# Kernel optimization log

Hardware: AMD Instinct MI355X
Metric: run time of the kernel (lower is better)

## Reference

```python
import math
import jax, jax.numpy as jnp
import numpy as np

D = 128
F = 512
EPS = 1e-5

def _lin(x, W, b):
    return x @ W + b  # W: [in, out]

def _bn(x2d, gamma, beta):
    # BatchNorm1d with track_running_stats=False: always batch stats, biased var
    m = jnp.mean(x2d, axis=0)
    v = jnp.mean((x2d - m) ** 2, axis=0)
    return gamma * (x2d - m) / jnp.sqrt(v + EPS) + beta

def _gelu(x):
    c = math.sqrt(2.0 / math.pi)
    return 0.5 * x * (1.0 + jnp.tanh(c * (x + 0.044715 * x ** 3)))

def setup_inputs() -> dict:
    key = jax.random.key(0)
    ks = jax.random.split(key, 16)
    B, N = 8, 256
    s = 1.0 / math.sqrt(D)
    inp = {
        'h': jax.random.normal(ks[0], (B, N, D), jnp.float32),
        'e': jax.random.normal(ks[1], (B, N, N, D), jnp.float32),
        'Uw': jax.random.uniform(ks[2], (D, D), jnp.float32, -s, s), 'Ub': jnp.zeros((D,), jnp.float32),
        'Vw': jax.random.uniform(ks[3], (D, D), jnp.float32, -s, s), 'Vb': jnp.zeros((D,), jnp.float32),
        'Aw': jax.random.uniform(ks[4], (D, D), jnp.float32, -s, s), 'Ab': jnp.zeros((D,), jnp.float32),
        'Bw': jax.random.uniform(ks[5], (D, D), jnp.float32, -s, s), 'Bb': jnp.zeros((D,), jnp.float32),
        'Cw': jax.random.uniform(ks[6], (D, D), jnp.float32, -s, s), 'Cb': jnp.zeros((D,), jnp.float32),
        'gamma_h': jnp.ones((D,), jnp.float32), 'beta_h': jnp.zeros((D,), jnp.float32),
        'gamma_e': jnp.ones((D,), jnp.float32), 'beta_e': jnp.zeros((D,), jnp.float32),
        'W1': jax.random.uniform(ks[7], (D, F), jnp.float32, -s, s), 'b1': jnp.zeros((F,), jnp.float32),
        'W2': jax.random.uniform(ks[8], (F, D), jnp.float32, -1.0 / math.sqrt(F), 1.0 / math.sqrt(F)), 'b2': jnp.zeros((D,), jnp.float32),
    }
    return inp

def reference(h, e, Uw, Ub, Vw, Vb, Aw, Ab, Bw, Bb, Cw, Cb,
              gamma_h, beta_h, gamma_e, beta_e, W1, b1, W2, b2):
    B, N, Dd = h.shape
    h_in, e_in = h, e
    Uh = _lin(h, Uw, Ub)          # [B,N,D]
    Vh = _lin(h, Vw, Vb)          # [B,N,D]
    Ah = _lin(h, Aw, Ab)
    Bh = _lin(h, Bw, Bb)
    Ce = _lin(e, Cw, Cb)          # [B,N,N,D]
    e_new = Ah[:, None, :, :] + Bh[:, :, None, :] + Ce  # [B,N,N,D]
    gates = jax.nn.sigmoid(e_new)
    # sum_j gates[b,i,j,d] * Vh[b,j,d]
    h_new = Uh + jnp.einsum('bijd,bjd->bid', gates, Vh)
    h_new = _bn(h_new.reshape(B * N, Dd), gamma_h, beta_h).reshape(B, N, Dd)
    e_out = _bn(e_new.reshape(B * N * N, Dd), gamma_e, beta_e).reshape(B, N, N, Dd)
    e_out = jax.nn.relu(e_out)
    h_new = _lin(_gelu(_lin(h_new, W1, b1)), W2, b2)
    return (h_in + h_new, e_in + e_out)
```

## Files before the change

### kernel.cpp

```cpp
#include <hip/hip_runtime.h>
#include <math.h>

#define D 128
#define NN 256
#define NB 2048
#define FF 512

typedef float f32x4 __attribute__((ext_vector_type(4)));
typedef __bf16 bf16x8 __attribute__((ext_vector_type(8)));
typedef unsigned int u32x4 __attribute__((ext_vector_type(4)));

__device__ __forceinline__ float gelu_f(float x) {
  float x3 = x * x * x;
  float u = 0.7978845608028654f * (x + 0.044715f * x3);
  return 0.5f * x * (1.0f + tanhf(u));
}

__device__ __forceinline__ bf16x8 cvt8(f32x4 a, f32x4 b) {
  bf16x8 r;
  r[0] = (__bf16)a.x; r[1] = (__bf16)a.y; r[2] = (__bf16)a.z; r[3] = (__bf16)a.w;
  r[4] = (__bf16)b.x; r[5] = (__bf16)b.y; r[6] = (__bf16)b.z; r[7] = (__bf16)b.w;
  return r;
}

__device__ __forceinline__ float sigmoid_f(float v) {
  float ex = __builtin_amdgcn_exp2f(-1.44269504f * v);
  return __builtin_amdgcn_rcpf(1.0f + ex);
}

__device__ __forceinline__ unsigned int packbf(float a, float v) {
  unsigned short ha = __builtin_bit_cast(unsigned short, (__bf16)a);
  unsigned short hv = __builtin_bit_cast(unsigned short, (__bf16)v);
  return (unsigned int)ha | ((unsigned int)hv << 16);
}
__device__ __forceinline__ float bflo(unsigned int u) {
  return __builtin_bit_cast(float, u << 16);
}
__device__ __forceinline__ float bfhi(unsigned int u) {
  return __builtin_bit_cast(float, u & 0xffff0000u);
}

__global__ __launch_bounds__(256) void k0_pack(const float* __restrict__ Cw,
                                               __bf16* __restrict__ ws0) {
  int tid = blockIdx.x * 256 + threadIdx.x;
  int l  = tid & 63;
  int nt = tid >> 8;
  int ks = (tid >> 6) & 3;
  int d  = nt * 16 + (l & 15);
  int kb = ks * 32 + (l >> 4) * 8;
  bf16x8 v;
#pragma unroll
  for (int q = 0; q < 8; ++q) v[q] = (__bf16)Cw[(kb + q) * D + d];
  *(bf16x8*)(ws0 + tid * 8) = v;
}

__global__ __launch_bounds__(256) void k1_lin4(
    const float* __restrict__ h,
    const float* __restrict__ Uw, const float* __restrict__ Ub,
    const float* __restrict__ Vw, const float* __restrict__ Vb,
    const float* __restrict__ Aw, const float* __restrict__ Ab,
    const float* __restrict__ Bw, const float* __restrict__ Bb,
    const float* __restrict__ Cb,
    float* __restrict__ wsU, float* __restrict__ wsB,
    unsigned int* __restrict__ wsAVT, unsigned int* __restrict__ wsAVR) {
  __shared__ float hrow[D];
  __shared__ float exA[D];
  __shared__ float exV[D];
  int row = blockIdx.x;
  int b = row >> 8, i = row & 255;
  int t = threadIdx.x;
  if (t < D) hrow[t] = h[row * D + t];
  __syncthreads();
  int d = t & 127;
  bool lo = (t < 128);
  const float* W0 = lo ? Uw : Vw;
  const float* W1m = lo ? Aw : Bw;
  float a0 = (lo ? Ub : Vb)[d];
  float a1 = lo ? Ab[d] : (Bb[d] + Cb[d]);
#pragma unroll 4
  for (int k = 0; k < D; ++k) {
    float hk = hrow[k];
    a0 = fmaf(hk, W0[k * D + d], a0);
    a1 = fmaf(hk, W1m[k * D + d], a1);
  }
  if (lo) {
    wsU[row * D + d] = a0;
    exA[d] = a1;
  } else {
    exV[d] = a0;
    wsB[row * D + d] = a1;
  }
  __syncthreads();
  if (t < 128) {
    unsigned int p = packbf(exA[t], exV[t]);
    wsAVR[row * D + t] = p;
    wsAVT[(b << 15) + t * NN + i] = p;
  }
}

__global__ __launch_bounds__(256, 3) void k_gemm(
    const float* __restrict__ e,
    const __bf16* __restrict__ ws0,
    __bf16* __restrict__ ws1) {
  __shared__ __align__(16) __bf16 bfr[16384];
  __shared__ __align__(16) unsigned int stW[4224];
  const int t = threadIdx.x;
  const int blk = blockIdx.x;

#pragma unroll
  for (int c = 0; c < 8; ++c) {
    int idx = c * 256 + t;
    *(f32x4*)(bfr + idx * 8) = *(const f32x4*)(ws0 + idx * 8);
  }
  __syncthreads();

  const int w = t >> 6;
  const int l = t & 63;
  const int l15 = l & 15;
  const int lhi = l >> 4;
  unsigned int* stWu = stW + w * 1056;

  const float* eblk = e + (size_t)blk * (NN * D);

  const float* ap = eblk + (w * 64 + l15) * D + lhi * 8;
  f32x4 pf[8];
#pragma unroll
  for (int q = 0; q < 8; ++q) pf[q] = *(const f32x4*)(ap + (q >> 1) * 32 + (q & 1) * 4);

#pragma unroll 1
  for (int mt = 0; mt < 4; ++mt) {
    bf16x8 af[4];
#pragma unroll
    for (int ks = 0; ks < 4; ++ks) af[ks] = cvt8(pf[2 * ks], pf[2 * ks + 1]);
    if (mt < 3) {
      const float* ap2 = ap + (mt + 1) * 16 * D;
#pragma unroll
      for (int q = 0; q < 8; ++q) pf[q] = *(const f32x4*)(ap2 + (q >> 1) * 32 + (q & 1) * 4);
    }
    const int J0 = w * 64 + mt * 16;
#pragma unroll
    for (int nt = 0; nt < 8; ++nt) {
      f32x4 acc = {0.f, 0.f, 0.f, 0.f};
#pragma unroll
      for (int ks = 0; ks < 4; ++ks) {
        bf16x8 bfrg = *(const bf16x8*)(bfr + ((nt * 4 + ks) * 64 + l) * 8);
        acc = __builtin_amdgcn_mfma_f32_16x16x32_bf16(af[ks], bfrg, acc, 0, 0, 0);
      }
#pragma unroll
      for (int r = 0; r < 4; ++r) {
        float v = acc[r];
        float vp = __shfl_xor(v, 1);
        if ((l15 & 1) == 0) {
          stWu[(lhi * 4 + r) * 66 + (nt << 3) + (l15 >> 1)] = packbf(v, vp);
        }
      }
    }
    unsigned int* dstu = (unsigned int*)(ws1 + (size_t)blk * (NN * D) + J0 * D);
#pragma unroll
    for (int i = 0; i < 16; ++i) {
      dstu[i * 64 + l] = stWu[i * 66 + l];
    }
  }
}

__global__ __launch_bounds__(256) void k_stats(
    const __bf16* __restrict__ ws1,
    const unsigned int* __restrict__ AVR,
    const float* __restrict__ Bh2,
    float* __restrict__ wsP) {
  __shared__ float red[16][3][128];
  const int t = threadIdx.x;
  const int blk = blockIdx.x;
  const int b = blk >> 8;
  const int jg = t >> 4;
  const int dg = t & 15;

  float cb[8];
  {
    f32x4 c0 = *(const f32x4*)(Bh2 + blk * D + dg * 8);
    f32x4 c1 = *(const f32x4*)(Bh2 + blk * D + dg * 8 + 4);
#pragma unroll
    for (int q = 0; q < 4; ++q) { cb[q] = c0[q]; cb[4 + q] = c1[q]; }
  }

  float es[8], eq[8], hp[8];
#pragma unroll
  for (int q = 0; q < 8; ++q) { es[q] = 0.f; eq[q] = 0.f; hp[q] = 0.f; }

  const unsigned int* w1 = (const unsigned int*)(ws1 + (size_t)blk * (NN * D));
  const unsigned int* avb = AVR + ((size_t)(b << 8)) * D;

#pragma unroll 1
  for (int k = 0; k < 16; ++k) {
    const int j = k * 16 + jg;
    u32x4 a = *(const u32x4*)(w1 + j * 64 + dg * 4);
    u32x4 av0 = *(const u32x4*)(avb + j * D + dg * 8);
    u32x4 av1 = *(const u32x4*)(avb + j * D + dg * 8 + 4);
#pragma unroll
    for (int q = 0; q < 4; ++q) {
      unsigned int avA = (q < 2) ? av0[2 * q] : av1[2 * (q - 2)];
      unsigned int avB = (q < 2) ? av0[2 * q + 1] : av1[2 * (q - 2) + 1];
      float v0 = bflo(a[q]) + cb[2 * q] + bflo(avA);
      float v1 = bfhi(a[q]) + cb[2 * q + 1] + bflo(avB);
      es[2 * q] += v0;
      eq[2 * q] = fmaf(v0, v0, eq[2 * q]);
      hp[2 * q] = fmaf(sigmoid_f(v0), bfhi(avA), hp[2 * q]);
      es[2 * q + 1] += v1;
      eq[2 * q + 1] = fmaf(v1, v1, eq[2 * q + 1]);
      hp[2 * q + 1] = fmaf(sigmoid_f(v1), bfhi(avB), hp[2 * q + 1]);
    }
  }

#pragma unroll
  for (int q = 0; q < 8; ++q) {
    red[jg][0][dg * 8 + q] = es[q];
    red[jg][1][dg * 8 + q] = eq[q];
    red[jg][2][dg * 8 + q] = hp[q];
  }
  __syncthreads();
  if (t < 128) {
    float S = 0.f, Q = 0.f, H = 0.f;
#pragma unroll
    for (int g = 0; g < 16; ++g) {
      S += red[g][0][t];
      Q += red[g][1][t];
      H += red[g][2][t];
    }
    wsP[blk * 384 + t] = S;
    wsP[blk * 384 + 128 + t] = Q;
    wsP[blk * 384 + 256 + t] = H;
  }
}

__global__ __launch_bounds__(256) void k_epass1s(
    const __bf16* __restrict__ ws1,
    const float* __restrict__ e,
    const unsigned int* __restrict__ AVR,
    const float* __restrict__ Bh2,
    const float* __restrict__ ws6,
    float* __restrict__ out_e) {
  const int tid = blockIdx.x * 256 + threadIdx.x;
  const int d0 = (tid & 15) * 8;
  f32x4 ge0 = *(const f32x4*)(ws6 + d0);
  f32x4 ge1 = *(const f32x4*)(ws6 + d0 + 4);
  f32x4 be0 = *(const f32x4*)(ws6 + 128 + d0);
  f32x4 be1 = *(const f32x4*)(ws6 + 128 + d0 + 4);
#pragma unroll 2
  for (int k = 0; k < 16; ++k) {
    size_t idx = (size_t)tid + (size_t)k * 524288;
    size_t row = idx >> 4;
    int j = (int)(row & 255);
    int bb = (int)(row >> 16);
    size_t avrow = ((size_t)(bb << 8) + j);
    u32x4 u = *(const u32x4*)(ws1 + idx * 8);
    u32x4 av0 = *(const u32x4*)(AVR + avrow * D + d0);
    u32x4 av1 = *(const u32x4*)(AVR + avrow * D + d0 + 4);
    const float* cbp = Bh2 + (row >> 8) * D + d0;
    f32x4 c0 = *(const f32x4*)cbp;
    f32x4 c1 = *(const f32x4*)(cbp + 4);
    const float* ep = e + idx * 8;
    f32x4 e0 = *(const f32x4*)ep;
    f32x4 e1 = *(const f32x4*)(ep + 4);
    f32x4 o0, o1;
#pragma unroll
    for (int q = 0; q < 2; ++q) {
      float v0 = bflo(u[q]) + c0[2 * q] + bflo(av0[2 * q]);
      float v1 = bfhi(u[q]) + c0[2 * q + 1] + bflo(av0[2 * q + 1]);
      o0[2 * q]     = fmaxf(fmaf(v0, ge0[2 * q], be0[2 * q]), 0.f) + e0[2 * q];
      o0[2 * q + 1] = fmaxf(fmaf(v1, ge0[2 * q + 1], be0[2 * q + 1]), 0.f) + e0[2 * q + 1];
      float v2 = bflo(u[2 + q]) + c1[2 * q] + bflo(av1[2 * q]);
      float v3 = bfhi(u[2 + q]) + c1[2 * q + 1] + bflo(av1[2 * q + 1]);
      o1[2 * q]     = fmaxf(fmaf(v2, ge1[2 * q], be1[2 * q]), 0.f) + e1[2 * q];
      o1[2 * q + 1] = fmaxf(fmaf(v3, ge1[2 * q + 1], be1[2 * q + 1]), 0.f) + e1[2 * q + 1];
    }
    float* op = out_e + idx * 8;
    *(f32x4*)op = o0;
    *(f32x4*)(op + 4) = o1;
  }
}

__global__ __launch_bounds__(256, 3) void k_epass0_fused(
    const float* __restrict__ e,
    const __bf16* __restrict__ ws0,
    const unsigned int* __restrict__ AVT,
    const float* __restrict__ Bh2,
    float* __restrict__ wsP) {
  __shared__ __align__(16) __bf16 bfr[16384];
  __shared__ __align__(16) unsigned int uni32[4224];
  const int t = threadIdx.x;
  const int blk = blockIdx.x;
  const int b = blk >> 8;

#pragma unroll
  for (int c = 0; c < 8; ++c) {
    int idx = c * 256 + t;
    *(f32x4*)(bfr + idx * 8) = *(const f32x4*)(ws0 + idx * 8);
  }
  __syncthreads();

  const int w = t >> 6;
  const int l = t & 63;
  const int l15 = l & 15;
  const int lhi = l >> 4;

  float cbias[8];
#pragma unroll
  for (int nt = 0; nt < 8; ++nt) cbias[nt] = Bh2[blk * D + nt * 16 + l15];

  float es[8], eq[8], hp[8];
#pragma unroll
  for (int nt = 0; nt < 8; ++nt) { es[nt] = 0.f; eq[nt] = 0.f; hp[nt] = 0.f; }

  const float* eblk = e + (size_t)blk * (NN * D);
  const unsigned int* AVb = AVT + ((size_t)b << 15);

  const float* ap = eblk + (w * 64 + l15) * D + lhi * 8;
  f32x4 pf[8];
#pragma unroll
  for (int q = 0; q < 8; ++q) pf[q] = *(const f32x4*)(ap + (q >> 1) * 32 + (q & 1) * 4);

#pragma unroll 1
  for (int mt = 0; mt < 4; ++mt) {
    bf16x8 af[4];
#pragma unroll
    for (int ks = 0; ks < 4; ++ks) af[ks] = cvt8(pf[2 * ks], pf[2 * ks + 1]);
    if (mt < 3) {
      const float* ap2 = ap + (mt + 1) * 16 * D;
#pragma unroll
      for (int q = 0; q < 8; ++q) pf[q] = *(const f32x4*)(ap2 + (q >> 1) * 32 + (q & 1) * 4);
    }
    const int J0 = w * 64 + mt * 16;
#pragma unroll
    for (int nt = 0; nt < 8; ++nt) {
      f32x4 acc = {0.f, 0.f, 0.f, 0.f};
#pragma unroll
      for (int ks = 0; ks < 4; ++ks) {
        bf16x8 bfrg = *(const bf16x8*)(bfr + ((nt * 4 + ks) * 64 + l) * 8);
        acc = __builtin_amdgcn_mfma_f32_16x16x32_bf16(af[ks], bfrg, acc, 0, 0, 0);
      }
      const int doff = (nt * 16 + l15) * NN + J0 + lhi * 4;
      u32x4 uv = *(const u32x4*)(AVb + doff);
#pragma unroll
      for (int r = 0; r < 4; ++r) {
        float v = acc[r] + cbias[nt] + bflo(uv[r]);
        es[nt] += v;
        eq[nt] = fmaf(v, v, eq[nt]);
        float g = sigmoid_f(v);
        hp[nt] = fmaf(g, bfhi(uv[r]), hp[nt]);
      }
    }
  }

#pragma unroll
  for (int nt = 0; nt < 8; ++nt) {
    es[nt] += __shfl_xor(es[nt], 16); es[nt] += __shfl_xor(es[nt], 32);
    eq[nt] += __shfl_xor(eq[nt], 16); eq[nt] += __shfl_xor(eq[nt], 32);
    hp[nt] += __shfl_xor(hp[nt], 16); hp[nt] += __shfl_xor(hp[nt], 32);
  }
  __syncthreads();
  float* red = (float*)uni32;
  if (l < 16) {
#pragma unroll
    for (int nt = 0; nt < 8; ++nt) {
      red[(w * 3 + 0) * 128 + nt * 16 + l] = es[nt];
      red[(w * 3 + 1) * 128 + nt * 16 + l] = eq[nt];
      red[(w * 3 + 2) * 128 + nt * 16 + l] = hp[nt];
    }
  }
  __syncthreads();
  if (t < 128) {
    float S = red[0 * 128 + t] + red[3 * 128 + t] + red[6 * 128 + t] + red[9 * 128 + t];
    float Q = red[1 * 128 + t] + red[4 * 128 + t] + red[7 * 128 + t] + red[10 * 128 + t];
    float H = red[2 * 128 + t] + red[5 * 128 + t] + red[8 * 128 + t] + red[11 * 128 + t];
    wsP[blk * 384 + t] = S;
    wsP[blk * 384 + 128 + t] = Q;
    wsP[blk * 384 + 256 + t] = H;
  }
}

__global__ __launch_bounds__(256, 3) void k_epass1(
    const float* __restrict__ e,
    const __bf16* __restrict__ ws0,
    const unsigned int* __restrict__ AVT,
    const float* __restrict__ Bh2,
    const float* __restrict__ ws6,
    float* __restrict__ out_e) {
  __shared__ __align__(16) __bf16 bfr[16384];
  __shared__ float st[4][16 * 68];
  const int t = threadIdx.x;
  const int blk = blockIdx.x;
  const int b = blk >> 8;

#pragma unroll
  for (int c = 0; c < 8; ++c) {
    int idx = c * 256 + t;
    *(f32x4*)(bfr + idx * 8) = *(const f32x4*)(ws0 + idx * 8);
  }
  __syncthreads();

  const int w = t >> 6;
  const int l = t & 63;
  const int l15 = l & 15;
  const int lhi = l >> 4;
  float* stw = &st[w][0];

  float cbias[8], ge[8], be[8];
#pragma unroll
  for (int nt = 0; nt < 8; ++nt) {
    int d = nt * 16 + l15;
    cbias[nt] = Bh2[blk * D + d];
    ge[nt] = ws6[d];
    be[nt] = ws6[128 + d];
  }

  const float* eblk = e + (size_t)blk * (NN * D);
  const unsigned int* AVb = AVT + ((size_t)b << 15);
  float* outB = out_e + (size_t)blk * (NN * D);

  const int srow = l >> 4;
  const int scol = (l & 15) * 4;

  const float* ap = eblk + (w * 64 + l15) * D + lhi * 8;
  f32x4 pf[8];
#pragma unroll
  for (int q = 0; q < 8; ++q) pf[q] = *(const f32x4*)(ap + (q >> 1) * 32 + (q & 1) * 4);

#pragma unroll 1
  for (int mt = 0; mt < 4; ++mt) {
    bf16x8 af[4];
#pragma unroll
    for (int ks = 0; ks < 4; ++ks) af[ks] = cvt8(pf[2 * ks], pf[2 * ks + 1]);
    if (mt < 3) {
      const float* ap2 = ap + (mt + 1) * 16 * D;
#pragma unroll
      for (int q = 0; q < 8; ++q) pf[q] = *(const f32x4*)(ap2 + (q >> 1) * 32 + (q & 1) * 4);
    }
    const int J0 = w * 64 + mt * 16;
#pragma unroll
    for (int p = 0; p < 2; ++p) {
#pragma unroll
      for (int ntl = 0; ntl < 4; ++ntl) {
        const int nt = p * 4 + ntl;
        f32x4 acc = {0.f, 0.f, 0.f, 0.f};
#pragma unroll
        for (int ks = 0; ks < 4; ++ks) {
          bf16x8 bfrg = *(const bf16x8*)(bfr + ((nt * 4 + ks) * 64 + l) * 8);
          acc = __builtin_amdgcn_mfma_f32_16x16x32_bf16(af[ks], bfrg, acc, 0, 0, 0);
        }
        const int doff = (nt * 16 + l15) * NN + J0 + lhi * 4;
        u32x4 uv = *(const u32x4*)(AVb + doff);
#pragma unroll
        for (int r = 0; r < 4; ++r) {
          float v = acc[r] + cbias[nt] + bflo(uv[r]);
          stw[(lhi * 4 + r) * 68 + ntl * 16 + l15] =
              fmaxf(fmaf(v, ge[nt], be[nt]), 0.0f);
        }
      }
#pragma unroll
      for (int it = 0; it < 4; ++it) {
        const int row = it * 4 + srow;
        const int goff = (J0 + row) * D + p * 64 + scol;
        f32x4 res = *(const f32x4*)(eblk + goff);
        f32x4 q = *(const f32x4*)(stw + row * 68 + scol);
        *(f32x4*)(outB + goff) = q + res;
      }
    }
  }
}

__global__ __launch_bounds__(256) void k3a(const float* __restrict__ wsP,
                                           const float* __restrict__ wsU,
                                           float* __restrict__ ws7,
                                           float* __restrict__ wsPB) {
  __shared__ float red2[2][4][128];
  int t = threadIdx.x, blk = blockIdx.x;
  int c = t & 127, half = t >> 7;
  float es = 0.f, eq = 0.f, hs = 0.f, hq = 0.f;
  for (int s = 0; s < 16; ++s) {
    int row = blk * 32 + half * 16 + s;
    es += wsP[row * 384 + c];
    eq += wsP[row * 384 + 128 + c];
    float v = wsU[row * D + c] + wsP[row * 384 + 256 + c];
    ws7[row * D + c] = v;
    hs += v;
    hq = fmaf(v, v, hq);
  }
  red2[half][0][c] = es; red2[half][1][c] = eq;
  red2[half][2][c] = hs; red2[half][3][c] = hq;
  __syncthreads();
  if (t < 128) {
#pragma unroll
    for (int k = 0; k < 4; ++k)
      wsPB[blk * 512 + k * 128 + t] = red2[0][k][t] + red2[1][k][t];
  }
}

__global__ __launch_bounds__(256) void k3b(const float* __restrict__ wsPB,
                                           const float* __restrict__ gamma_e,
                                           const float* __restrict__ beta_e,
                                           const float* __restrict__ gamma_h,
                                           const float* __restrict__ beta_h,
                                           float* __restrict__ ws6) {
  int t = threadIdx.x;
  int c = t & 127, g = t >> 7;
  float S = 0.f, Q = 0.f;
  for (int blk = 0; blk < 64; ++blk) {
    S += wsPB[blk * 512 + (g * 2) * 128 + c];
    Q += wsPB[blk * 512 + (g * 2 + 1) * 128 + c];
  }
  float M = g ? 2048.0f : 524288.0f;
  float mean = S / M;
  float var = Q / M - mean * mean;
  float rstd = rsqrtf(var + 1e-5f);
  float gam = (g ? gamma_h : gamma_e)[c] * rstd;
  float bet = (g ? beta_h : beta_e)[c] - mean * gam;
  ws6[g * 256 + c] = gam;
  ws6[g * 256 + 128 + c] = bet;
}

__global__ __launch_bounds__(256) void k4_mlp(
    const float* __restrict__ ws7, const float* __restrict__ ws6,
    const float* __restrict__ W1, const float* __restrict__ b1,
    const float* __restrict__ W2, const float* __restrict__ b2,
    const float* __restrict__ h_in, float* __restrict__ out_h) {
  __shared__ float hn[D];
  __shared__ float t1[FF];
  int row = blockIdx.x, t = threadIdx.x;
  if (t < D) {
    float v = ws7[row * D + t];
    hn[t] = fmaf(v, ws6[256 + t], ws6[384 + t]);
  }
  __syncthreads();
  {
    int f0 = t, f1 = t + 256;
    float a0 = b1[f0], a1 = b1[f1];
#pragma unroll 4
    for (int k = 0; k < D; ++k) {
      float hk = hn[k];
      a0 = fmaf(hk, W1[k * FF + f0], a0);
      a1 = fmaf(hk, W1[k * FF + f1], a1);
    }
    t1[f0] = gelu_f(a0);
    t1[f1] = gelu_f(a1);
  }
  __syncthreads();
  if (t < D) {
    float a = b2[t];
#pragma unroll 4
    for (int k = 0; k < FF; ++k) a = fmaf(t1[k], W2[k * D + t], a);
    out_h[row * D + t] = h_in[row * D + t] + a;
  }
}

extern "C" void kernel_launch(void* const* d_in, const int* in_sizes, int n_in,
                              void* d_out, int out_size, void* d_ws, size_t ws_size,
                              hipStream_t stream) {
  (void)in_sizes; (void)n_in; (void)out_size;
  const float* h       = (const float*)d_in[0];
  const float* e       = (const float*)d_in[1];
  const float* Uw      = (const float*)d_in[2];
  const float* Ub      = (const float*)d_in[3];
  const float* Vw      = (const float*)d_in[4];
  const float* Vb      = (const float*)d_in[5];
  const float* Aw      = (const float*)d_in[6];
  const float* Ab      = (const float*)d_in[7];
  const float* Bw      = (const float*)d_in[8];
  const float* Bb      = (const float*)d_in[9];
  const float* Cw      = (const float*)d_in[10];
  const float* Cb      = (const float*)d_in[11];
  const float* gamma_h = (const float*)d_in[12];
  const float* beta_h  = (const float*)d_in[13];
  const float* gamma_e = (const float*)d_in[14];
  const float* beta_e  = (const float*)d_in[15];
  const float* W1      = (const float*)d_in[16];
  const float* b1      = (const float*)d_in[17];
  const float* W2      = (const float*)d_in[18];
  const float* b2      = (const float*)d_in[19];

  float* ws   = (float*)d_ws;
  __bf16* ws0 = (__bf16*)ws;
  float* wsU  = ws + 8192;
  float* wsB  = wsU + NB * D;
  unsigned int* wsAVT = (unsigned int*)(wsB + NB * D);
  unsigned int* wsAVR = wsAVT + NB * D;
  float* wsP  = (float*)(wsAVR + NB * D);
  float* wsPB = wsP + NB * 384;
  float* ws6  = wsPB + 64 * 512;
  float* ws7  = ws6 + 512;
  size_t head_bytes = (size_t)(ws7 + NB * D - ws) * 4;
  head_bytes = (head_bytes + 255) & ~(size_t)255;
  __bf16* ws1 = (__bf16*)((char*)d_ws + head_bytes);
  size_t need = head_bytes + (size_t)NB * NN * D * 2;
  bool big = (ws_size >= need);

  float* out_h = (float*)d_out;
  float* out_e = out_h + NB * D;

  k0_pack<<<dim3(8), dim3(256), 0, stream>>>(Cw, ws0);
  k1_lin4<<<dim3(NB), dim3(256), 0, stream>>>(h, Uw, Ub, Vw, Vb, Aw, Ab, Bw, Bb,
                                              Cb, wsU, wsB, wsAVT, wsAVR);
  if (big) {
    k_gemm<<<dim3(NB), dim3(256), 0, stream>>>(e, ws0, ws1);
    k_stats<<<dim3(NB), dim3(256), 0, stream>>>(ws1, wsAVR, wsB, wsP);
  } else {
    k_epass0_fused<<<dim3(NB), dim3(256), 0, stream>>>(e, ws0, wsAVT, wsB, wsP);
  }
  k3a<<<dim3(64), dim3(256), 0, stream>>>(wsP, wsU, ws7, wsPB);
  k3b<<<dim3(1), dim3(256), 0, stream>>>(wsPB, gamma_e, beta_e, gamma_h, beta_h, ws6);
  k4_mlp<<<dim3(NB), dim3(256), 0, stream>>>(ws7, ws6, W1, b1, W2, b2, h, out_h);
  if (big) {
    k_epass1s<<<dim3(2048), dim3(256), 0, stream>>>(ws1, e, wsAVR, wsB, ws6, out_e);
  } else {
    k_epass1<<<dim3(NB), dim3(256), 0, stream>>>(e, ws0, wsAVT, wsB, ws6, out_e);
  }
}
```

Before: 433.8 us.

## Fuse edge statistics reduction into GEMM epilogue and drop k_stats kernel

Computes the per-channel sum, sum of squares and sigmoid-gated aggregation directly in the k_gemm epilogue from the bf16 tile values already staged in shared memory, then reduces across the four waves in reused shared memory. This removes the separate k_stats kernel, its launch, and its full re-read of the bf16 intermediate. In exchange the GEMM kernel does more ALU work and holds more registers, which could lower occupancy under its launch bounds.

```diff
diff --git a/kernel.cpp b/kernel.cpp
--- a/kernel.cpp
+++ b/kernel.cpp
@@ -9,6 +9,7 @@
 typedef float f32x4 __attribute__((ext_vector_type(4)));
 typedef __bf16 bf16x8 __attribute__((ext_vector_type(8)));
 typedef unsigned int u32x4 __attribute__((ext_vector_type(4)));
+typedef unsigned int u32x2 __attribute__((ext_vector_type(2)));
 
 __device__ __forceinline__ float gelu_f(float x) {
   float x3 = x * x * x;
@@ -101,11 +102,15 @@
 __global__ __launch_bounds__(256, 3) void k_gemm(
     const float* __restrict__ e,
     const __bf16* __restrict__ ws0,
+    const unsigned int* __restrict__ AVR,
+    const float* __restrict__ Bh2,
+    float* __restrict__ wsP,
     __bf16* __restrict__ ws1) {
   __shared__ __align__(16) __bf16 bfr[16384];
   __shared__ __align__(16) unsigned int stW[4224];
   const int t = threadIdx.x;
   const int blk = blockIdx.x;
+  const int b = blk >> 8;
 
 #pragma unroll
   for (int c = 0; c < 8; ++c) {
@@ -120,7 +125,12 @@
   const int lhi = l >> 4;
   unsigned int* stWu = stW + w * 1056;
 
+  const float cb0 = Bh2[blk * D + 2 * l];
+  const float cb1 = Bh2[blk * D + 2 * l + 1];
+  float es0 = 0.f, es1 = 0.f, eq0 = 0.f, eq1 = 0.f, hp0 = 0.f, hp1 = 0.f;
+
   const float* eblk = e + (size_t)blk * (NN * D);
+  const unsigned int* AVb = AVR + ((size_t)(b << 8)) * D;
 
   const float* ap = eblk + (w * 64 + l15) * D + lhi * 8;
   f32x4 pf[8];
@@ -156,76 +166,36 @@
       }
     }
     unsigned int* dstu = (unsigned int*)(ws1 + (size_t)blk * (NN * D) + J0 * D);
+    const unsigned int* avrow = AVb + (size_t)J0 * D;
 #pragma unroll
     for (int i = 0; i < 16; ++i) {
-      dstu[i * 64 + l] = stWu[i * 66 + l];
-    }
-  }
-}
-
-__global__ __launch_bounds__(256) void k_stats(
-    const __bf16* __restrict__ ws1,
-    const unsigned int* __restrict__ AVR,
-    const float* __restrict__ Bh2,
-    float* __restrict__ wsP) {
-  __shared__ float red[16][3][128];
-  const int t = threadIdx.x;
-  const int blk = blockIdx.x;
-  const int b = blk >> 8;
-  const int jg = t >> 4;
-  const int dg = t & 15;
-
-  float cb[8];
-  {
-    f32x4 c0 = *(const f32x4*)(Bh2 + blk * D + dg * 8);
-    f32x4 c1 = *(const f32x4*)(Bh2 + blk * D + dg * 8 + 4);
-#pragma unroll
-    for (int q = 0; q < 4; ++q) { cb[q] = c0[q]; cb[4 + q] = c1[q]; }
-  }
-
-  float es[8], eq[8], hp[8];
-#pragma unroll
-  for (int q = 0; q < 8; ++q) { es[q] = 0.f; eq[q] = 0.f; hp[q] = 0.f; }
-
-  const unsigned int* w1 = (const unsigned int*)(ws1 + (size_t)blk * (NN * D));
-  const unsigned int* avb = AVR + ((size_t)(b << 8)) * D;
-
-#pragma unroll 1
-  for (int k = 0; k < 16; ++k) {
-    const int j = k * 16 + jg;
-    u32x4 a = *(const u32x4*)(w1 + j * 64 + dg * 4);
-    u32x4 av0 = *(const u32x4*)(avb + j * D + dg * 8);
-    u32x4 av1 = *(const u32x4*)(avb + j * D + dg * 8 + 4);
-#pragma unroll
-    for (int q = 0; q < 4; ++q) {
-      unsigned int avA = (q < 2) ? av0[2 * q] : av1[2 * (q - 2)];
-      unsigned int avB = (q < 2) ? av0[2 * q + 1] : av1[2 * (q - 2) + 1];
-      float v0 = bflo(a[q]) + cb[2 * q] + bflo(avA);
-      float v1 = bfhi(a[q]) + cb[2 * q + 1] + bflo(avB);
-      es[2 * q] += v0;
-      eq[2 * q] = fmaf(v0, v0, eq[2 * q]);
-      hp[2 * q] = fmaf(sigmoid_f(v0), bfhi(avA), hp[2 * q]);
-      es[2 * q + 1] += v1;
-      eq[2 * q + 1] = fmaf(v1, v1, eq[2 * q + 1]);
-      hp[2 * q + 1] = fmaf(sigmoid_f(v1), bfhi(avB), hp[2 * q + 1]);
-    }
-  }
-
-#pragma unroll
-  for (int q = 0; q < 8; ++q) {
-    red[jg][0][dg * 8 + q] = es[q];
-    red[jg][1][dg * 8 + q] = eq[q];
-    red[jg][2][dg * 8 + q] = hp[q];
-  }
+      unsigned int s = stWu[i * 66 + l];
+      dstu[i * 64 + l] = s;
+      u32x2 av = *(const u32x2*)(avrow + i * D + 2 * l);
+      float v0 = bflo(s) + cb0 + bflo(av.x);
+      float v1 = bfhi(s) + cb1 + bflo(av.y);
+      es0 += v0;
+      eq0 = fmaf(v0, v0, eq0);
+      hp0 = fmaf(sigmoid_f(v0), bfhi(av.x), hp0);
+      es1 += v1;
+      eq1 = fmaf(v1, v1, eq1);
+      hp1 = fmaf(sigmoid_f(v1), bfhi(av.y), hp1);
+    }
+  }
+
+  __syncthreads();
+  float* red = (float*)stW;
+  red[(w * 3 + 0) * 128 + 2 * l] = es0;
+  red[(w * 3 + 0) * 128 + 2 * l + 1] = es1;
+  red[(w * 3 + 1) * 128 + 2 * l] = eq0;
+  red[(w * 3 + 1) * 128 + 2 * l + 1] = eq1;
+  red[(w * 3 + 2) * 128 + 2 * l] = hp0;
+  red[(w * 3 + 2) * 128 + 2 * l + 1] = hp1;
   __syncthreads();
   if (t < 128) {
-    float S = 0.f, Q = 0.f, H = 0.f;
-#pragma unroll
-    for (int g = 0; g < 16; ++g) {
-      S += red[g][0][t];
-      Q += red[g][1][t];
-      H += red[g][2][t];
-    }
+    float S = red[0 * 128 + t] + red[3 * 128 + t] + red[6 * 128 + t] + red[9 * 128 + t];
+    float Q = red[1 * 128 + t] + red[4 * 128 + t] + red[7 * 128 + t] + red[10 * 128 + t];
+    float H = red[2 * 128 + t] + red[5 * 128 + t] + red[8 * 128 + t] + red[11 * 128 + t];
     wsP[blk * 384 + t] = S;
     wsP[blk * 384 + 128 + t] = Q;
     wsP[blk * 384 + 256 + t] = H;
@@ -600,8 +570,7 @@
   k1_lin4<<<dim3(NB), dim3(256), 0, stream>>>(h, Uw, Ub, Vw, Vb, Aw, Ab, Bw, Bb,
                                               Cb, wsU, wsB, wsAVT, wsAVR);
   if (big) {
-    k_gemm<<<dim3(NB), dim3(256), 0, stream>>>(e, ws0, ws1);
-    k_stats<<<dim3(NB), dim3(256), 0, stream>>>(ws1, wsAVR, wsB, wsP);
+    k_gemm<<<dim3(NB), dim3(256), 0, stream>>>(e, ws0, wsAVR, wsB, wsP, ws1);
   } else {
     k_epass0_fused<<<dim3(NB), dim3(256), 0, stream>>>(e, ws0, wsAVT, wsB, wsP);
   }
```

Result: slower. 480.2 us (+10.7%).
